# Performance work log

Measured on AMD Instinct MI355X. Metric: run time of the kernel, lower is better.

Reference implementation:

```python
import jax, jax.numpy as jnp
import numpy as np

H = 16      # heads
D = 64      # head_dim
C = 64      # k_centroid
HID = H * D
TAU1 = 1.0
TAU2 = 1.0


def setup_inputs() -> dict:
    key = jax.random.key(0)
    ks = jax.random.split(key, 12)
    B, S = 4, 1024
    inv = 1.0 / np.sqrt(D)
    return {
        "query": jax.random.normal(ks[0], (B, S, HID), dtype=jnp.float32),
        "key": jax.random.normal(ks[1], (B, S, HID), dtype=jnp.float32),
        "value": jax.random.normal(ks[2], (B, S, HID), dtype=jnp.float32),
        "Wq": jax.random.uniform(ks[3], (D, D), jnp.float32, -inv, inv),
        "bq": jax.random.uniform(ks[4], (D,), jnp.float32, -inv, inv),
        "Wk": jax.random.uniform(ks[5], (D, D), jnp.float32, -inv, inv),
        "bk": jax.random.uniform(ks[6], (D,), jnp.float32, -inv, inv),
        "Wv": jax.random.uniform(ks[7], (D, D), jnp.float32, -inv, inv),
        "bv": jax.random.uniform(ks[8], (D,), jnp.float32, -inv, inv),
        "centroid": jax.random.uniform(ks[9], (D, C), jnp.float32, -0.5, 0.5),
        "Wfc": jax.random.uniform(ks[10], (HID, HID), jnp.float32, -1.0 / np.sqrt(HID), 1.0 / np.sqrt(HID)),
        "bfc": jax.random.uniform(ks[11], (HID,), jnp.float32, -1.0 / np.sqrt(HID), 1.0 / np.sqrt(HID)),
    }


def _forward(query, key, value, Wq, bq, Wk, bk, Wv, bv, centroid, Wfc, bfc):
    B, S, _ = query.shape
    q = query.reshape(B, S, H, D)
    k = key.reshape(B, S, H, D)
    v = value.reshape(B, S, H, D)
    # per-head linear projections (applied on last dim, nn.Linear equivalent)
    Q = jnp.einsum('nshd,de->nshe', q, Wq) + bq
    K = jnp.einsum('nshd,de->nshe', k, Wk) + bk
    V = jnp.einsum('nshd,de->nshe', v, Wv) + bv
    # VQ-style key quantization: project keys onto centroids, gumbel-softmax over codebook
    K_ = jnp.einsum('nshd,dc->nshc', K, centroid)            # [B,S,H,C]
    g1 = jax.random.gumbel(jax.random.key(42), K_.shape, dtype=K_.dtype)
    prob = jax.nn.softmax((K_ + g1) / TAU1, axis=-1)
    sto_K = jnp.einsum('nshc,dc->nshd', prob, centroid)      # prob @ centroid.T
    # gumbel-softmax attention over QK^T
    scores = jnp.einsum('nqhd,nkhd->nhqk', Q, sto_K)         # [B,H,S,S]
    g2 = jax.random.gumbel(jax.random.key(43), scores.shape, dtype=scores.dtype)
    attn = jax.nn.softmax((scores + g2) / TAU2, axis=3)
    out = jnp.einsum('nhql,nlhd->nqhd', attn, V).reshape(B, S, HID)
    return jnp.einsum('nsd,de->nse', out, Wfc) + bfc


def reference(query, key, value, Wq, bq, Wk, bk, Wv, bv, centroid, Wfc, bfc):
    return _forward(query, key, value, Wq, bq, Wk, bk, Wv, bv, centroid, Wfc, bfc)
```

## Files before the change

### kernel.cpp

```cpp
#include <hip/hip_runtime.h>
#include <hip/hip_bf16.h>
#include <cstdint>

typedef unsigned short u16;
typedef __attribute__((ext_vector_type(8))) short short8;
typedef __attribute__((ext_vector_type(4))) float f32x4;

#define LT 72
#define LOG2E 1.4426950408889634f

__device__ __forceinline__ u16 f2bf(float x) {
  __hip_bfloat16 h = __float2bfloat16(x);
  union { __hip_bfloat16 h; u16 u; } cv; cv.h = h; return cv.u;
}
__device__ __forceinline__ u16 f2bf_fast(float x) {
  uint32_t b = __float_as_uint(x);
  return (u16)((b + 0x7fffu + ((b >> 16) & 1u)) >> 16);
}
__device__ __forceinline__ float bf2f(u16 u) {
  union { u16 u; __hip_bfloat16 h; } cv; cv.u = u; return __bfloat162float(cv.h);
}
__device__ __forceinline__ float ld(const void* base, size_t i, int isb) {
  return isb ? bf2f(((const u16*)base)[i]) : ((const float*)base)[i];
}
__device__ __forceinline__ void st_out(void* base, size_t i, float v, int isb) {
  if (isb) ((u16*)base)[i] = f2bf_fast(v);
  else     ((float*)base)[i] = v;
}
__device__ __forceinline__ int probe_is_bf16(const void* q) {
  const u16* u = (const u16*)q;
  int sane = 0;
  for (int i = 0; i < 64; i++) {
    u16 x = u[2 * i];
    int e = (x >> 7) & 0xff;
    sane += (int)(((e >= 117) && (e <= 133)) || ((x & 0x7fff) == 0));
  }
  return sane >= 32;
}

__device__ __forceinline__ uint32_t rotl32(uint32_t x, int n) {
  return __builtin_amdgcn_alignbit(x, x, (uint32_t)(32 - n));
}
__device__ __forceinline__ void threefry4x(uint32_t k1, uint32_t x1base,
                                           uint32_t out[4]) {
  const uint32_t ks2 = k1 ^ 0x1BD11BDAu;
  uint32_t x0[4], x1[4];
  #pragma unroll
  for (int j = 0; j < 4; j++) { x0[j] = 0u; x1[j] = x1base + ((uint32_t)j << 4); }
#define R4(rot) \
  _Pragma("unroll") \
  for (int j = 0; j < 4; j++) { \
    x0[j] += x1[j]; x1[j] = rotl32(x1[j], rot); x1[j] ^= x0[j]; \
  }
  R4(13) R4(15) R4(26) R4(6)
  #pragma unroll
  for (int j = 0; j < 4; j++) { x0[j] += k1; x1[j] += ks2 + 1u; }
  R4(17) R4(29) R4(16) R4(24)
  #pragma unroll
  for (int j = 0; j < 4; j++) { x0[j] += ks2; x1[j] += 2u; }
  R4(13) R4(15) R4(26) R4(6)
  #pragma unroll
  for (int j = 0; j < 4; j++) { x1[j] += k1 + 3u; }
  R4(17) R4(29) R4(16) R4(24)
  #pragma unroll
  for (int j = 0; j < 4; j++) { x0[j] += k1; x1[j] += ks2 + 4u; }
  R4(13) R4(15) R4(26) R4(6)
  #pragma unroll
  for (int j = 0; j < 4; j++) { out[j] = (x0[j] + ks2) ^ (x1[j] + 5u); }
#undef R4
}
__device__ __forceinline__ float rcp_l2n(uint32_t bits) {
  float u = __uint_as_float(0x3f800000u | (bits >> 9)) - 1.0f;
  float l2n = -__log2f(u);
  float t = 1.0f - u;
  float fix = fmaf(0.5f * t, t, t) * LOG2E;
  l2n = (bits >= 0xFF000000u) ? fix : l2n;
  return __builtin_amdgcn_rcpf(l2n);
}
__device__ __forceinline__ float qsum(float v) {
  v += __shfl_xor(v, 1, 64);
  v += __shfl_xor(v, 2, 64);
  v += __shfl_xor(v, 4, 64);
  v += __shfl_xor(v, 8, 64);
  return v;
}
__device__ __forceinline__ void stage_tile(u16* dst, const u16* src,
                                           int src_stride, int tid) {
  #pragma unroll
  for (int i = 0; i < 2; i++) {
    int u = tid + (i << 8);
    int r = u >> 3, c8 = (u & 7) * 8;
    *(short8*)&dst[r * LT + c8] =
        *(const short8*)&src[(size_t)r * src_stride + c8];
  }
}
__device__ __forceinline__ void pf_tile(short8 regs[2], const u16* src,
                                        int src_stride, int tid) {
  #pragma unroll
  for (int i = 0; i < 2; i++) {
    int u = tid + (i << 8);
    int r = u >> 3, c8 = (u & 7) * 8;
    regs[i] = *(const short8*)&src[(size_t)r * src_stride + c8];
  }
}
__device__ __forceinline__ void flush_tile(u16* dst, const short8 regs[2],
                                           int tid) {
  #pragma unroll
  for (int i = 0; i < 2; i++) {
    int u = tid + (i << 8);
    int r = u >> 3, c8 = (u & 7) * 8;
    *(short8*)&dst[r * LT + c8] = regs[i];
  }
}
__device__ __forceinline__ void stage_x(u16* dst, const void* src, size_t base,
                                        int isb, int tid) {
  if (isb) {
    const u16* s = (const u16*)src;
    #pragma unroll
    for (int i = 0; i < 2; i++) {
      int u = tid + (i << 8);
      int r = u >> 3, c8 = (u & 7) * 8;
      *(short8*)&dst[r * LT + c8] =
          *(const short8*)&s[base + (size_t)r * 1024 + c8];
    }
  } else {
    const float* s = (const float*)src;
    #pragma unroll
    for (int i = 0; i < 4; i++) {
      int f = (tid + (i << 8)) << 2;
      int r = f >> 6, c = f & 63;
      float4 v = *(const float4*)&s[base + (size_t)r * 1024 + c];
      ushort4 w4 = {f2bf_fast(v.x), f2bf_fast(v.y), f2bf_fast(v.z),
                    f2bf_fast(v.w)};
      *(ushort4*)&dst[r * LT + c] = w4;
    }
  }
}
__device__ __forceinline__ void gemm16(const u16* A, const u16* Bt, int w,
                                       int qd, int n, f32x4 acc[4]) {
  short8 a0 = *(const short8*)&A[(16 * w + n) * LT + qd * 8];
  short8 a1 = *(const short8*)&A[(16 * w + n) * LT + qd * 8 + 32];
  #pragma unroll
  for (int ct = 0; ct < 4; ct++) {
    short8 b0 = *(const short8*)&Bt[(16 * ct + n) * LT + qd * 8];
    short8 b1 = *(const short8*)&Bt[(16 * ct + n) * LT + qd * 8 + 32];
    acc[ct] = __builtin_amdgcn_mfma_f32_16x16x32_bf16(a0, b0, acc[ct], 0, 0, 0);
    acc[ct] = __builtin_amdgcn_mfma_f32_16x16x32_bf16(a1, b1, acc[ct], 0, 0, 0);
  }
}

__global__ __launch_bounds__(256, 4) void prep_kernel(
    const void* query, const void* Wq, const void* Wk, const void* Wv,
    const void* cen, const void* Wfc,
    const void* bq, const void* bk, const void* bv, const void* bfc,
    u16* WqT, u16* WkT, u16* WvT, u16* cenT, u16* cenN, u16* WfcT,
    float* biasF, int* flagp) {
  __shared__ __align__(16) u16 T[64 * LT];
  __shared__ int sflag;
  int tid = threadIdx.x, bid = blockIdx.x;
  if (tid == 0) sflag = probe_is_bf16(query);
  __syncthreads();
  int isb = sflag;

  if (bid < 256) {
    int k0 = (bid >> 4) * 64, c0 = (bid & 15) * 64;
    if (isb) {
      const u16* s = (const u16*)Wfc;
      #pragma unroll
      for (int i = 0; i < 2; i++) {
        int u = tid + (i << 8);
        int r = u >> 3, c8 = (u & 7) * 8;
        short8 v = *(const short8*)&s[(size_t)(k0 + r) * 1024 + c0 + c8];
        #pragma unroll
        for (int e = 0; e < 8; e++) T[(c8 + e) * LT + r] = (u16)v[e];
      }
    } else {
      const float* s = (const float*)Wfc;
      #pragma unroll
      for (int i = 0; i < 4; i++) {
        int f = (tid + (i << 8)) << 2;
        int r = f >> 6, c = f & 63;
        float4 v = *(const float4*)&s[(size_t)(k0 + r) * 1024 + c0 + c];
        T[(c + 0) * LT + r] = f2bf(v.x);
        T[(c + 1) * LT + r] = f2bf(v.y);
        T[(c + 2) * LT + r] = f2bf(v.z);
        T[(c + 3) * LT + r] = f2bf(v.w);
      }
    }
    __syncthreads();
    #pragma unroll
    for (int i = 0; i < 2; i++) {
      int u = tid + (i << 8);
      int cr = u >> 3, k8 = (u & 7) * 8;
      *(short8*)&WfcT[(size_t)(c0 + cr) * 1024 + k0 + k8] =
          *(const short8*)&T[cr * LT + k8];
    }
  } else if (bid < 259) {
    const void* W = (bid == 256) ? Wq : ((bid == 257) ? Wk : Wv);
    u16* WT = (bid == 256) ? WqT : ((bid == 257) ? WkT : WvT);
    float scl = (bid == 256) ? LOG2E : 1.0f;
    #pragma unroll
    for (int i = 0; i < 16; i++) {
      int f = tid + (i << 8);
      int r = f >> 6, c = f & 63;
      T[c * LT + r] = f2bf(ld(W, f, isb) * scl);
    }
    __syncthreads();
    #pragma unroll
    for (int i = 0; i < 16; i++) {
      int f = tid + (i << 8);
      WT[f] = T[(f >> 6) * LT + (f & 63)];
    }
  } else if (bid == 259) {
    #pragma unroll
    for (int i = 0; i < 16; i++) {
      int f = tid + (i << 8);
      int d = f >> 6, c = f & 63;
      float v = ld(cen, f, isb);
      cenN[f] = f2bf(v);
      T[c * LT + d] = f2bf(v * LOG2E);
    }
    __syncthreads();
    #pragma unroll
    for (int i = 0; i < 16; i++) {
      int f = tid + (i << 8);
      cenT[f] = T[(f >> 6) * LT + (f & 63)];
    }
  } else {
    if (tid < 64) {
      biasF[tid] = ld(bq, tid, isb) * LOG2E;
      biasF[64 + tid] = ld(bk, tid, isb);
      biasF[128 + tid] = ld(bv, tid, isb);
    }
    #pragma unroll
    for (int j = 0; j < 4; j++) {
      int c = tid + (j << 8);
      biasF[192 + c] = ld(bfc, c, isb);
    }
    if (tid == 0) *flagp = isb;
  }
}

__global__ __launch_bounds__(256, 4) void proj_kernel(
    const void* q_in, const void* k_in, const void* v_in,
    const u16* WqT, const u16* WkT, const u16* WvT,
    const u16* cenT, const u16* cenN, const float* biasF, const int* flagp,
    u16* Qbf, u16* Kbf, u16* VTbf) {
  __shared__ __align__(16) u16 XB[64 * LT], WB[64 * LT], CT[64 * LT], CN[64 * LT];
  int tid = threadIdx.x;
  int w = tid >> 6, ln = tid & 63, qd = ln >> 4, n = ln & 15;
  int bh = blockIdx.x >> 4, st = blockIdx.x & 15;
  int b = bh >> 4, h = bh & 15, s0 = st * 64;
  int isb = *flagp;
  size_t xbase = ((size_t)(b * 1024 + s0)) * 1024 + h * 64;
  size_t obase = (size_t)bh * 65536 + (size_t)s0 * 64;
  f32x4 z = {0.f, 0.f, 0.f, 0.f};

  stage_tile(CT, cenT, 64, tid);
  stage_tile(CN, cenN, 64, tid);
  stage_tile(WB, WqT, 64, tid);
  stage_x(XB, q_in, xbase, isb, tid);
  __syncthreads();

  {
    f32x4 acc[4] = {z, z, z, z};
    gemm16(XB, WB, w, qd, n, acc);
    #pragma unroll
    for (int ct = 0; ct < 4; ct++) {
      int col = 16 * ct + n;
      float bia = biasF[col];
      #pragma unroll
      for (int i = 0; i < 4; i++) {
        int srow = 16 * w + 4 * qd + i;
        Qbf[obase + (size_t)srow * 64 + col] = f2bf_fast(acc[ct][i] + bia);
      }
    }
  }
  __syncthreads();
  stage_tile(WB, WkT, 64, tid);
  stage_x(XB, k_in, xbase, isb, tid);
  __syncthreads();

  {
    f32x4 acc[4] = {z, z, z, z};
    gemm16(XB, WB, w, qd, n, acc);
    #pragma unroll
    for (int ct = 0; ct < 4; ct++) {
      int col = 16 * ct + n;
      float bia = biasF[64 + col];
      #pragma unroll
      for (int i = 0; i < 4; i++)
        XB[(16 * w + 4 * qd + i) * LT + col] = f2bf_fast(acc[ct][i] + bia);
    }
    f32x4 kc[4] = {z, z, z, z};
    gemm16(XB, CT, w, qd, n, kc);
    __syncthreads();
    uint32_t idxb42 = (((((uint32_t)b << 10) |
                         (uint32_t)(s0 + 16 * w + 4 * qd)) << 10) |
                       ((uint32_t)h << 6) | (uint32_t)n) + 42u;
    float lsum[4];
    #pragma unroll
    for (int i = 0; i < 4; i++) {
      uint32_t r[4];
      threefry4x(42u, idxb42 + ((uint32_t)i << 10), r);
      float ps = 0.f;
      #pragma unroll
      for (int ct = 0; ct < 4; ct++) {
        float pv = __builtin_amdgcn_exp2f(kc[ct][i]) * rcp_l2n(r[ct]);
        ps += pv;
        WB[(16 * w + 4 * qd + i) * LT + 16 * ct + n] = f2bf_fast(pv);
      }
      lsum[i] = qsum(ps);
    }
    f32x4 sk[4] = {z, z, z, z};
    gemm16(WB, CN, w, qd, n, sk);
    #pragma unroll
    for (int i = 0; i < 4; i++) {
      float inv = __builtin_amdgcn_rcpf(lsum[i]);
      int srow = 16 * w + 4 * qd + i;
      #pragma unroll
      for (int ct = 0; ct < 4; ct++)
        Kbf[obase + (size_t)srow * 64 + 16 * ct + n] =
            f2bf_fast(sk[ct][i] * inv);
    }
  }
  __syncthreads();
  stage_tile(WB, WvT, 64, tid);
  stage_x(XB, v_in, xbase, isb, tid);
  __syncthreads();

  {
    f32x4 acc[4] = {z, z, z, z};
    gemm16(XB, WB, w, qd, n, acc);
    #pragma unroll
    for (int ct = 0; ct < 4; ct++) {
      int col = 16 * ct + n;
      float bia = biasF[128 + col];
      #pragma unroll
      for (int i = 0; i < 4; i++)
        CT[col * LT + 16 * w + 4 * qd + i] = f2bf_fast(acc[ct][i] + bia);
    }
    __syncthreads();
    #pragma unroll
    for (int i = 0; i < 2; i++) {
      int u = tid + (i << 8);
      int dr = u >> 3, c8 = (u & 7) * 8;
      *(short8*)&VTbf[(size_t)bh * 65536 + (size_t)dr * 1024 + s0 + c8] =
          *(const short8*)&CT[dr * LT + c8];
    }
  }
}

__global__ __launch_bounds__(256, 4) void attn_kernel(
    const u16* __restrict__ Qbf, const u16* __restrict__ Kbf,
    const u16* __restrict__ VTbf, u16* __restrict__ AObf) {
  __shared__ __align__(16) u16 QS[64 * LT], KS[64 * LT], VS[64 * LT], PS[64 * LT];
  int tid = threadIdx.x;
  int w = tid >> 6, ln = tid & 63, qd = ln >> 4, n = ln & 15;
  int bh = blockIdx.x >> 4, qt = blockIdx.x & 15;
  int b = bh >> 4, h = bh & 15, q0 = qt * 64;
  f32x4 z = {0.f, 0.f, 0.f, 0.f};
  const u16* Kb = Kbf + (size_t)bh * 65536;
  const u16* Vb = VTbf + (size_t)bh * 65536;

  stage_tile(QS, Qbf + (size_t)bh * 65536 + (size_t)q0 * 64, 64, tid);

  f32x4 o[4] = {z, z, z, z};
  float lsum[4] = {0.f, 0.f, 0.f, 0.f};
  uint32_t idxb43 = (((uint32_t)bh << 20) |
                     ((uint32_t)(q0 + 16 * w + 4 * qd) << 10) | (uint32_t)n) +
                    43u;

  short8 kreg[2], vreg[2];
  pf_tile(kreg, Kb, 64, tid);
  pf_tile(vreg, Vb, 1024, tid);

  for (int lt = 0; lt < 16; lt++) {
    float rnl[4][4];
    uint32_t base43 = idxb43 + ((uint32_t)lt << 6);
    #pragma unroll
    for (int i = 0; i < 4; i++) {
      uint32_t r[4];
      threefry4x(43u, base43 + ((uint32_t)i << 10), r);
      #pragma unroll
      for (int ct = 0; ct < 4; ct++) rnl[i][ct] = rcp_l2n(r[ct]);
    }

    __syncthreads();
    flush_tile(KS, kreg, tid);
    flush_tile(VS, vreg, tid);
    if (lt < 15) {
      pf_tile(kreg, Kb + (size_t)(lt + 1) * 4096, 64, tid);
      pf_tile(vreg, Vb + (lt + 1) * 64, 1024, tid);
    }
    __syncthreads();

    f32x4 sc[4] = {z, z, z, z};
    gemm16(QS, KS, w, qd, n, sc);

    #pragma unroll
    for (int i = 0; i < 4; i++) {
      #pragma unroll
      for (int ct = 0; ct < 4; ct++) {
        float p = __builtin_amdgcn_exp2f(sc[ct][i]) * rnl[i][ct];
        lsum[i] += p;
        PS[(16 * w + 4 * qd + i) * LT + 16 * ct + n] = f2bf_fast(p);
      }
    }
    gemm16(PS, VS, w, qd, n, o);
  }

  #pragma unroll
  for (int i = 0; i < 4; i++) {
    float inv = __builtin_amdgcn_rcpf(qsum(lsum[i]));
    int qrow = q0 + 16 * w + 4 * qd + i;
    size_t rb = ((size_t)(b * 1024 + qrow)) * 1024 + h * 64;
    #pragma unroll
    for (int ct = 0; ct < 4; ct++)
      AObf[rb + 16 * ct + n] = f2bf_fast(o[ct][i] * inv);
  }
}

__global__ __launch_bounds__(256, 4) void fc_kernel(
    const u16* __restrict__ AObf, const u16* __restrict__ WfcT,
    const float* __restrict__ biasF, const int* flagp, void* __restrict__ out) {
  __shared__ __align__(16) u16 AS[64 * LT], WS[64 * LT];
  int tid = threadIdx.x;
  int w = tid >> 6, ln = tid & 63, qd = ln >> 4, n = ln & 15;
  int r0 = (blockIdx.x >> 4) * 64, c0 = (blockIdx.x & 15) * 64;
  int isb = *flagp;
  f32x4 z = {0.f, 0.f, 0.f, 0.f};
  f32x4 acc[4] = {z, z, z, z};
  const u16* Ab = AObf + (size_t)r0 * 1024;
  const u16* Wb = WfcT + (size_t)c0 * 1024;

  short8 areg[2], wreg[2];
  pf_tile(areg, Ab, 1024, tid);
  pf_tile(wreg, Wb, 1024, tid);

  for (int kt = 0; kt < 16; kt++) {
    __syncthreads();
    flush_tile(AS, areg, tid);
    flush_tile(WS, wreg, tid);
    if (kt < 15) {
      pf_tile(areg, Ab + (kt + 1) * 64, 1024, tid);
      pf_tile(wreg, Wb + (kt + 1) * 64, 1024, tid);
    }
    __syncthreads();
    gemm16(AS, WS, w, qd, n, acc);
  }
  const float* bfcF = biasF + 192;
  #pragma unroll
  for (int ct = 0; ct < 4; ct++) {
    int col = c0 + 16 * ct + n;
    float bia = bfcF[col];
    #pragma unroll
    for (int i = 0; i < 4; i++) {
      int row = r0 + 16 * w + 4 * qd + i;
      st_out(out, (size_t)row * 1024 + col, acc[ct][i] + bia, isb);
    }
  }
}

extern "C" void kernel_launch(void* const* d_in, const int* in_sizes, int n_in,
                              void* d_out, int out_size, void* d_ws,
                              size_t ws_size, hipStream_t stream) {
  (void)in_sizes; (void)n_in; (void)out_size; (void)ws_size;
  const void* query = d_in[0];
  const void* key   = d_in[1];
  const void* value = d_in[2];
  const void* Wq = d_in[3]; const void* bq = d_in[4];
  const void* Wk = d_in[5]; const void* bk = d_in[6];
  const void* Wv = d_in[7]; const void* bv = d_in[8];
  const void* cen = d_in[9];
  const void* Wfc = d_in[10]; const void* bfc = d_in[11];

  u16* ws = (u16*)d_ws;
  u16* Qbf  = ws;
  u16* Kbf  = Qbf + 4194304;
  u16* VTbf = Kbf + 4194304;
  u16* AObf = VTbf + 4194304;
  u16* WfcT = AObf + 4194304;
  u16* WqTp = WfcT + 1048576;
  u16* WkTp = WqTp + 4096;
  u16* WvTp = WkTp + 4096;
  u16* cenTp = WvTp + 4096;
  u16* cenNp = cenTp + 4096;
  float* biasF = (float*)(cenNp + 4096);
  int* flagp = (int*)(biasF + 1216);

  prep_kernel<<<261, 256, 0, stream>>>(query, Wq, Wk, Wv, cen, Wfc, bq, bk, bv,
                                       bfc, WqTp, WkTp, WvTp, cenTp, cenNp,
                                       WfcT, biasF, flagp);
  proj_kernel<<<1024, 256, 0, stream>>>(query, key, value, WqTp, WkTp, WvTp,
                                        cenTp, cenNp, biasF, flagp,
                                        Qbf, Kbf, VTbf);
  attn_kernel<<<1024, 256, 0, stream>>>(Qbf, Kbf, VTbf, AObf);
  fc_kernel<<<1024, 256, 0, stream>>>(AObf, WfcT, biasF, flagp, d_out);
}
```

Baseline: 302.5 us.

## Split attention over key halves with combine pass; keep Q/A operands in registers

Attention is split along the key dimension into two halves, doubling the block count, and each half writes partial normalized outputs plus row sums. A new combine kernel merges the halves with sum-based weights. Q fragments are loaded straight into registers and P reuses the K shared buffer, which cuts LDS use and raises the occupancy hint to 6. fc_kernel also loads A fragments directly from global memory instead of staging them in LDS. The cost is an extra kernel launch, extra global traffic for the partials, an added barrier per tile, and one more bf16 rounding step.

```diff
diff --git a/kernel.cpp b/kernel.cpp
--- a/kernel.cpp
+++ b/kernel.cpp
@@ -140,6 +140,16 @@
                                        int qd, int n, f32x4 acc[4]) {
   short8 a0 = *(const short8*)&A[(16 * w + n) * LT + qd * 8];
   short8 a1 = *(const short8*)&A[(16 * w + n) * LT + qd * 8 + 32];
+  #pragma unroll
+  for (int ct = 0; ct < 4; ct++) {
+    short8 b0 = *(const short8*)&Bt[(16 * ct + n) * LT + qd * 8];
+    short8 b1 = *(const short8*)&Bt[(16 * ct + n) * LT + qd * 8 + 32];
+    acc[ct] = __builtin_amdgcn_mfma_f32_16x16x32_bf16(a0, b0, acc[ct], 0, 0, 0);
+    acc[ct] = __builtin_amdgcn_mfma_f32_16x16x32_bf16(a1, b1, acc[ct], 0, 0, 0);
+  }
+}
+__device__ __forceinline__ void gemm16r(short8 a0, short8 a1, const u16* Bt,
+                                        int qd, int n, f32x4 acc[4]) {
   #pragma unroll
   for (int ct = 0; ct < 4; ct++) {
     short8 b0 = *(const short8*)&Bt[(16 * ct + n) * LT + qd * 8];
@@ -351,19 +361,26 @@
   }
 }
 
-__global__ __launch_bounds__(256, 4) void attn_kernel(
+__global__ __launch_bounds__(256, 6) void attn_kernel(
     const u16* __restrict__ Qbf, const u16* __restrict__ Kbf,
-    const u16* __restrict__ VTbf, u16* __restrict__ AObf) {
-  __shared__ __align__(16) u16 QS[64 * LT], KS[64 * LT], VS[64 * LT], PS[64 * LT];
+    const u16* __restrict__ VTbf, u16* __restrict__ OhA, u16* __restrict__ OhB,
+    float* __restrict__ LsA, float* __restrict__ LsB) {
+  __shared__ __align__(16) u16 KS[64 * LT], VS[64 * LT];
+  u16* PS = KS;
   int tid = threadIdx.x;
   int w = tid >> 6, ln = tid & 63, qd = ln >> 4, n = ln & 15;
-  int bh = blockIdx.x >> 4, qt = blockIdx.x & 15;
+  int blk = blockIdx.x;
+  int bh = blk >> 5, half = (blk >> 4) & 1, qt = blk & 15;
   int b = bh >> 4, h = bh & 15, q0 = qt * 64;
   f32x4 z = {0.f, 0.f, 0.f, 0.f};
   const u16* Kb = Kbf + (size_t)bh * 65536;
   const u16* Vb = VTbf + (size_t)bh * 65536;
-
-  stage_tile(QS, Qbf + (size_t)bh * 65536 + (size_t)q0 * 64, 64, tid);
+  int lt0 = half * 8;
+
+  const u16* Qr = Qbf + ((size_t)bh << 16) +
+                  (size_t)(q0 + 16 * w + n) * 64 + qd * 8;
+  short8 qa0 = *(const short8*)Qr;
+  short8 qa1 = *(const short8*)(Qr + 32);
 
   f32x4 o[4] = {z, z, z, z};
   float lsum[4] = {0.f, 0.f, 0.f, 0.f};
@@ -372,10 +389,11 @@
                     43u;
 
   short8 kreg[2], vreg[2];
-  pf_tile(kreg, Kb, 64, tid);
-  pf_tile(vreg, Vb, 1024, tid);
-
-  for (int lt = 0; lt < 16; lt++) {
+  pf_tile(kreg, Kb + (size_t)lt0 * 4096, 64, tid);
+  pf_tile(vreg, Vb + lt0 * 64, 1024, tid);
+
+  for (int t = 0; t < 8; t++) {
+    int lt = lt0 + t;
     float rnl[4][4];
     uint32_t base43 = idxb43 + ((uint32_t)lt << 6);
     #pragma unroll
@@ -389,14 +407,15 @@
     __syncthreads();
     flush_tile(KS, kreg, tid);
     flush_tile(VS, vreg, tid);
-    if (lt < 15) {
+    if (t < 7) {
       pf_tile(kreg, Kb + (size_t)(lt + 1) * 4096, 64, tid);
       pf_tile(vreg, Vb + (lt + 1) * 64, 1024, tid);
     }
     __syncthreads();
 
     f32x4 sc[4] = {z, z, z, z};
-    gemm16(QS, KS, w, qd, n, sc);
+    gemm16r(qa0, qa1, KS, qd, n, sc);
+    __syncthreads();
 
     #pragma unroll
     for (int i = 0; i < 4; i++) {
@@ -410,44 +429,72 @@
     gemm16(PS, VS, w, qd, n, o);
   }
 
+  u16* Oh = half ? OhB : OhA;
+  float* Ls = half ? LsB : LsA;
   #pragma unroll
   for (int i = 0; i < 4; i++) {
-    float inv = __builtin_amdgcn_rcpf(qsum(lsum[i]));
+    float s = qsum(lsum[i]);
+    float inv = __builtin_amdgcn_rcpf(s);
     int qrow = q0 + 16 * w + 4 * qd + i;
     size_t rb = ((size_t)(b * 1024 + qrow)) * 1024 + h * 64;
     #pragma unroll
     for (int ct = 0; ct < 4; ct++)
-      AObf[rb + 16 * ct + n] = f2bf_fast(o[ct][i] * inv);
-  }
+      Oh[rb + 16 * ct + n] = f2bf_fast(o[ct][i] * inv);
+    if (n == 0) Ls[(bh << 10) + qrow] = s;
+  }
+}
+
+__global__ __launch_bounds__(256, 8) void combine_kernel(
+    const u16* __restrict__ OhA, const u16* __restrict__ OhB,
+    const float* __restrict__ LsA, const float* __restrict__ LsB,
+    u16* __restrict__ AObf) {
+  int idx = blockIdx.x * 256 + threadIdx.x;
+  int r = idx >> 7, cc = (idx & 127) << 3;
+  int h = cc >> 6, b = r >> 10, qrow = r & 1023;
+  int li = (((b << 4) | h) << 10) + qrow;
+  float lA = LsA[li], lB = LsB[li];
+  float rs = __builtin_amdgcn_rcpf(lA + lB);
+  float wA = lA * rs, wB = lB * rs;
+  size_t base = (size_t)r * 1024 + cc;
+  short8 a = *(const short8*)&OhA[base];
+  short8 bb = *(const short8*)&OhB[base];
+  short8 o;
+  #pragma unroll
+  for (int e = 0; e < 8; e++)
+    o[e] = (short)f2bf_fast(bf2f((u16)a[e]) * wA + bf2f((u16)bb[e]) * wB);
+  *(short8*)&AObf[base] = o;
 }
 
 __global__ __launch_bounds__(256, 4) void fc_kernel(
     const u16* __restrict__ AObf, const u16* __restrict__ WfcT,
     const float* __restrict__ biasF, const int* flagp, void* __restrict__ out) {
-  __shared__ __align__(16) u16 AS[64 * LT], WS[64 * LT];
+  __shared__ __align__(16) u16 WS[64 * LT];
   int tid = threadIdx.x;
   int w = tid >> 6, ln = tid & 63, qd = ln >> 4, n = ln & 15;
   int r0 = (blockIdx.x >> 4) * 64, c0 = (blockIdx.x & 15) * 64;
   int isb = *flagp;
   f32x4 z = {0.f, 0.f, 0.f, 0.f};
   f32x4 acc[4] = {z, z, z, z};
-  const u16* Ab = AObf + (size_t)r0 * 1024;
   const u16* Wb = WfcT + (size_t)c0 * 1024;
-
-  short8 areg[2], wreg[2];
-  pf_tile(areg, Ab, 1024, tid);
+  const u16* Ar = AObf + (size_t)(r0 + 16 * w + n) * 1024 + qd * 8;
+
+  short8 wreg[2];
   pf_tile(wreg, Wb, 1024, tid);
+  short8 a0 = *(const short8*)Ar;
+  short8 a1 = *(const short8*)(Ar + 32);
 
   for (int kt = 0; kt < 16; kt++) {
     __syncthreads();
-    flush_tile(AS, areg, tid);
     flush_tile(WS, wreg, tid);
+    if (kt < 15) pf_tile(wreg, Wb + (kt + 1) * 64, 1024, tid);
+    __syncthreads();
+    short8 na0, na1;
     if (kt < 15) {
-      pf_tile(areg, Ab + (kt + 1) * 64, 1024, tid);
-      pf_tile(wreg, Wb + (kt + 1) * 64, 1024, tid);
-    }
-    __syncthreads();
-    gemm16(AS, WS, w, qd, n, acc);
+      na0 = *(const short8*)(Ar + (kt + 1) * 64);
+      na1 = *(const short8*)(Ar + (kt + 1) * 64 + 32);
+    }
+    gemm16r(a0, a1, WS, qd, n, acc);
+    a0 = na0; a1 = na1;
   }
   const float* bfcF = biasF + 192;
   #pragma unroll
@@ -488,6 +535,10 @@
   u16* cenNp = cenTp + 4096;
   float* biasF = (float*)(cenNp + 4096);
   int* flagp = (int*)(biasF + 1216);
+  u16* OhA = ws + 17848832;
+  u16* OhB = OhA + 4194304;
+  float* LsA = (float*)(OhB + 4194304);
+  float* LsB = LsA + 65536;
 
   prep_kernel<<<261, 256, 0, stream>>>(query, Wq, Wk, Wv, cen, Wfc, bq, bk, bv,
                                        bfc, WqTp, WkTp, WvTp, cenTp, cenNp,
@@ -495,6 +546,7 @@
   proj_kernel<<<1024, 256, 0, stream>>>(query, key, value, WqTp, WkTp, WvTp,
                                         cenTp, cenNp, biasF, flagp,
                                         Qbf, Kbf, VTbf);
-  attn_kernel<<<1024, 256, 0, stream>>>(Qbf, Kbf, VTbf, AObf);
+  attn_kernel<<<2048, 256, 0, stream>>>(Qbf, Kbf, VTbf, OhA, OhB, LsA, LsB);
+  combine_kernel<<<2048, 256, 0, stream>>>(OhA, OhB, LsA, LsB, AObf);
   fc_kernel<<<1024, 256, 0, stream>>>(AObf, WfcT, biasF, flagp, d_out);
 }
```

Result: slower. 321.1 us (+6.2%).
